# Optimization experiments

Hardware: AMD Instinct MI355X
Metric: run time of the kernel (lower is better)

Reference implementation:

```python
import jax, jax.numpy as jnp
import numpy as np

N_NODES = 10000
N_EDGES = 320000
D_IN = 256
D_OUT = 256
MAX_NORM = 0.95

def setup_inputs() -> dict:
    key = jax.random.key(0)
    ks = jax.random.split(key, 7)
    x = jax.random.normal(ks[0], (N_NODES, D_IN), dtype=jnp.float32)
    edge_index = jax.random.randint(ks[1], (2, N_EDGES), 0, N_NODES, dtype=jnp.int64)
    # xavier-ish scales
    W = jax.random.normal(ks[2], (D_OUT, D_IN), dtype=jnp.float32) * (1.0 / np.sqrt(D_IN))
    b = jax.random.normal(ks[3], (D_OUT,), dtype=jnp.float32) * 0.02
    mag_w = jax.random.normal(ks[4], (1, D_IN), dtype=jnp.float32) * 0.02
    mag_b = jax.random.normal(ks[5], (1,), dtype=jnp.float32) * 0.02
    attn_w = jax.random.normal(ks[6], (1, 2 * D_OUT), dtype=jnp.float32) * (1.0 / np.sqrt(2 * D_OUT))
    return {"x": x, "edge_index": edge_index, "W": W, "b": b,
            "mag_w": mag_w, "mag_b": mag_b, "attn_w": attn_w}

def _expmap0(u):
    # Poincare ball exp map at origin, curvature c = 1.0
    un = jnp.linalg.norm(u, axis=-1, keepdims=True)
    un_c = jnp.maximum(un, 1e-15)
    return jnp.tanh(un_c) * u / un_c

def reference(x, edge_index, W, b, mag_w, mag_b, attn_w):
    N = x.shape[0]
    F_out = W.shape[0]
    # linear transform + directional/magnitude decomposition
    h_raw = x @ W.T + b                                              # (N, F)
    h_dir = h_raw / jnp.maximum(jnp.linalg.norm(h_raw, axis=-1, keepdims=True), 1e-12)
    h_mag = jax.nn.sigmoid(x @ mag_w.T + mag_b) * 1.5                # (N, 1)
    h = h_dir * h_mag                                                # (N, F)
    src, tgt = edge_index[0], edge_index[1]
    h_src = h[src]                                                   # (E, F)
    h_tgt = h[tgt]                                                   # (E, F)
    # attn(cat([h_src, h_tgt])) == h_src @ a_s + h_tgt @ a_t (avoids concat)
    a_s, a_t = attn_w[0, :F_out], attn_w[0, F_out:]
    scores = h_src @ a_s + h_tgt @ a_t                               # (E,)
    # scatter softmax over edges grouped by target node
    mx = jnp.maximum(jax.ops.segment_max(scores, tgt, num_segments=N), -1e9)
    ex = jnp.exp(scores - mx[tgt])
    se = jax.ops.segment_sum(ex, tgt, num_segments=N)
    attn_weights = ex / (se[tgt] + 1e-10)                            # (E,)
    # weighted message aggregation
    agg = jax.ops.segment_sum(h_src * attn_weights[:, None], tgt, num_segments=N)
    h_combined = h + agg
    h_poincare = _expmap0(h_combined)
    norms = jnp.linalg.norm(h_poincare, axis=1, keepdims=True)
    return jnp.where(norms > MAX_NORM, h_poincare * (MAX_NORM / (norms + 1e-8)), h_poincare)
```

## Files before the change

kernel.cpp:

```cpp
#include <hip/hip_runtime.h>
#include <math.h>

#define N_NODES 10000
#define N_EDGES 320000
#define D 256
#define CAP 128
#define BM 32
#define LDK 40
#define GB_GEMM ((N_NODES + BM - 1) / BM)
#define GB_BUILD ((N_EDGES + 255) / 256)

typedef __attribute__((ext_vector_type(8))) short short8;
typedef __attribute__((ext_vector_type(4))) float f32x4;

__device__ __forceinline__ ushort f2bf(float f) {
    union { float f; unsigned u; } v; v.f = f;
    unsigned r = v.u + 0x7FFFu + ((v.u >> 16) & 1u);
    return (ushort)(r >> 16);
}
__device__ __forceinline__ float bf2f(ushort u) {
    union { unsigned u; float f; } v; v.u = (unsigned)u << 16;
    return v.f;
}

__global__ __launch_bounds__(256) void k_prep(const float* __restrict__ W,
                                              ushort* __restrict__ Wb,
                                              unsigned* __restrict__ deg) {
    const int tid = blockIdx.x * 256 + threadIdx.x;
    const int i = tid * 4;
    const float4 v = *(const float4*)&W[i];
    ushort4 o;
    o.x = f2bf(v.x); o.y = f2bf(v.y); o.z = f2bf(v.z); o.w = f2bf(v.w);
    *(ushort4*)&Wb[i] = o;
    if (tid < N_NODES) deg[tid] = 0u;
}

__global__ __launch_bounds__(256) void k_main(const float* __restrict__ x,
                                              const ushort* __restrict__ Wb,
                                              const float* __restrict__ b,
                                              const float* __restrict__ mag_w,
                                              const float* __restrict__ mag_b,
                                              const float* __restrict__ attn_w,
                                              const int* __restrict__ ei,
                                              unsigned* __restrict__ deg,
                                              int* __restrict__ csr_src,
                                              ushort* __restrict__ hb,
                                              float* __restrict__ es) {
    if (blockIdx.x >= GB_GEMM) {
        const int e = (blockIdx.x - GB_GEMM) * 256 + threadIdx.x;
        if (e < N_EDGES) {
            int src = ei[e];
            int tgt = ei[N_EDGES + e];
            src = min(max(src, 0), N_NODES - 1);
            tgt = min(max(tgt, 0), N_NODES - 1);
            const unsigned slot = atomicAdd(&deg[tgt], 1u);
            if (slot < CAP) csr_src[(size_t)tgt * CAP + slot] = src;
        }
        return;
    }

    __shared__ ushort ldsA[2][BM * LDK];
    __shared__ ushort ldsB[2][256 * LDK];
    __shared__ float red_ssq[4][BM], red_ra[4][BM];
    __shared__ float smrow[BM], scl[BM];

    const int t = threadIdx.x;
    const int w = t >> 6, l = t & 63;
    const int bm = blockIdx.x * BM;
    const int sra = t >> 3, ka = (t & 7) * 4;
    const int am = bm + sra;
    const int srb = t >> 2, kb = (t & 3) * 8;
    const int fl = l & 15;
    const int fh = (l >> 4) * 8;
    const int rq = (l >> 4) * 4;

    f32x4 acc[2][4];
#pragma unroll
    for (int r = 0; r < 2; ++r)
#pragma unroll
        for (int c = 0; c < 4; ++c) acc[r][c] = (f32x4)(0.f);
    float sm_part = 0.f;

    float4 xa;
    short8 bv[4];

    {
        xa = make_float4(0.f, 0.f, 0.f, 0.f);
        if (am < N_NODES) xa = *(const float4*)&x[(size_t)am * D + ka];
        const float4 mwv = *(const float4*)&mag_w[ka];
        sm_part += xa.x * mwv.x + xa.y * mwv.y + xa.z * mwv.z + xa.w * mwv.w;
#pragma unroll
        for (int p = 0; p < 4; ++p)
            bv[p] = *(const short8*)&Wb[(size_t)(p * 64 + srb) * D + kb];
        ushort4 av;
        av.x = f2bf(xa.x); av.y = f2bf(xa.y); av.z = f2bf(xa.z); av.w = f2bf(xa.w);
        *(ushort4*)&ldsA[0][sra * LDK + ka] = av;
#pragma unroll
        for (int p = 0; p < 4; ++p)
            *(short8*)&ldsB[0][(p * 64 + srb) * LDK + kb] = bv[p];
    }
    __syncthreads();

    int cur = 0;
    for (int k0 = 32; k0 < D; k0 += 32) {
        xa = make_float4(0.f, 0.f, 0.f, 0.f);
        if (am < N_NODES) xa = *(const float4*)&x[(size_t)am * D + k0 + ka];
        const float4 mwv = *(const float4*)&mag_w[k0 + ka];
        sm_part += xa.x * mwv.x + xa.y * mwv.y + xa.z * mwv.z + xa.w * mwv.w;
#pragma unroll
        for (int p = 0; p < 4; ++p)
            bv[p] = *(const short8*)&Wb[(size_t)(p * 64 + srb) * D + k0 + kb];

        short8 af[2], bfr[4];
#pragma unroll
        for (int r = 0; r < 2; ++r)
            af[r] = *(short8*)&ldsA[cur][(r * 16 + fl) * LDK + fh];
#pragma unroll
        for (int c = 0; c < 4; ++c)
            bfr[c] = *(short8*)&ldsB[cur][(w * 64 + c * 16 + fl) * LDK + fh];
#pragma unroll
        for (int r = 0; r < 2; ++r)
#pragma unroll
            for (int c = 0; c < 4; ++c)
                acc[r][c] = __builtin_amdgcn_mfma_f32_16x16x32_bf16(af[r], bfr[c], acc[r][c], 0, 0, 0);

        ushort4 av;
        av.x = f2bf(xa.x); av.y = f2bf(xa.y); av.z = f2bf(xa.z); av.w = f2bf(xa.w);
        *(ushort4*)&ldsA[cur ^ 1][sra * LDK + ka] = av;
#pragma unroll
        for (int p = 0; p < 4; ++p)
            *(short8*)&ldsB[cur ^ 1][(p * 64 + srb) * LDK + kb] = bv[p];
        __syncthreads();
        cur ^= 1;
    }
    {
        short8 af[2], bfr[4];
#pragma unroll
        for (int r = 0; r < 2; ++r)
            af[r] = *(short8*)&ldsA[cur][(r * 16 + fl) * LDK + fh];
#pragma unroll
        for (int c = 0; c < 4; ++c)
            bfr[c] = *(short8*)&ldsB[cur][(w * 64 + c * 16 + fl) * LDK + fh];
#pragma unroll
        for (int r = 0; r < 2; ++r)
#pragma unroll
            for (int c = 0; c < 4; ++c)
                acc[r][c] = __builtin_amdgcn_mfma_f32_16x16x32_bf16(af[r], bfr[c], acc[r][c], 0, 0, 0);
    }

#pragma unroll
    for (int o = 1; o < 8; o <<= 1) sm_part += __shfl_xor(sm_part, o);
    if ((t & 7) == 0) smrow[sra] = sm_part;

    float bn[4], asn[4];
#pragma unroll
    for (int c = 0; c < 4; ++c) {
        const int n = w * 64 + c * 16 + fl;
        bn[c]  = b[n];
        asn[c] = attn_w[n];
    }

#pragma unroll
    for (int r = 0; r < 2; ++r) {
#pragma unroll
        for (int reg = 0; reg < 4; ++reg) {
            float vssq = 0.f, vra = 0.f;
#pragma unroll
            for (int c = 0; c < 4; ++c) {
                const float v = acc[r][c][reg] + bn[c];
                vssq += v * v;
                vra  += v * asn[c];
            }
#pragma unroll
            for (int o = 1; o < 16; o <<= 1) {
                vssq += __shfl_xor(vssq, o);
                vra  += __shfl_xor(vra, o);
            }
            if (fl == 0) {
                const int m = r * 16 + rq + reg;
                red_ssq[w][m] = vssq;
                red_ra[w][m]  = vra;
            }
        }
    }
    __syncthreads();

    if (t < BM) {
        const int gm = bm + t;
        const float ssq = red_ssq[0][t] + red_ssq[1][t] + red_ssq[2][t] + red_ssq[3][t];
        const float ra  = red_ra[0][t]  + red_ra[1][t]  + red_ra[2][t]  + red_ra[3][t];
        const float norm = sqrtf(ssq);
        const float mag  = 1.5f / (1.f + expf(-(smrow[t] + mag_b[0])));
        const float scale = mag / fmaxf(norm, 1e-12f);
        scl[t] = scale;
        if (gm < N_NODES) es[gm] = expf(ra * scale);
    }
    __syncthreads();

#pragma unroll
    for (int r = 0; r < 2; ++r) {
#pragma unroll
        for (int reg = 0; reg < 4; ++reg) {
            const int ml = r * 16 + rq + reg;
            const int m = bm + ml;
            if (m < N_NODES) {
                const float scale = scl[ml];
#pragma unroll
                for (int c = 0; c < 4; ++c) {
                    const int n = w * 64 + c * 16 + fl;
                    hb[(size_t)m * D + n] = f2bf((acc[r][c][reg] + bn[c]) * scale);
                }
            }
        }
    }
}

__global__ __launch_bounds__(256) void k_agg(const ushort* __restrict__ hb,
                                             const unsigned* __restrict__ deg,
                                             const int* __restrict__ csr_src,
                                             const float* __restrict__ es,
                                             float* __restrict__ out) {
    const int wv = threadIdx.x >> 6;
    const int n = blockIdx.x * 4 + wv;
    const int lane = threadIdx.x & 63;
    const int d = min((int)deg[n], CAP);
    const size_t cbase = (size_t)n * CAP;

    int src0 = 0, src1 = 0;
    float w0 = 0.f, w1 = 0.f;
    if (lane < d)      { src0 = csr_src[cbase + lane];      w0 = es[src0]; }
    if (lane + 64 < d) { src1 = csr_src[cbase + lane + 64]; w1 = es[src1]; }
    float sum = w0 + w1;
#pragma unroll
    for (int o = 32; o > 0; o >>= 1) sum += __shfl_xor(sum, o);
    const float inv = 1.f / (sum + 1e-10f);

    const int coff = lane * 4;
    float4 A0 = make_float4(0.f, 0.f, 0.f, 0.f), A1 = A0, A2 = A0, A3 = A0;

    {
        const int cnt = min(d, 64);
        int e = 0;
        for (; e + 8 <= cnt; e += 8) {
            int s[8]; float q[8]; ushort4 v[8];
#pragma unroll
            for (int j = 0; j < 8; ++j) { s[j] = __shfl(src0, e + j); q[j] = __shfl(w0, e + j); }
#pragma unroll
            for (int j = 0; j < 8; ++j) v[j] = *(const ushort4*)&hb[(size_t)s[j] * D + coff];
#pragma unroll
            for (int j = 0; j < 8; ++j) {
                float4* A = (j & 2) ? ((j & 1) ? &A3 : &A2) : ((j & 1) ? &A1 : &A0);
                A->x += q[j] * bf2f(v[j].x); A->y += q[j] * bf2f(v[j].y);
                A->z += q[j] * bf2f(v[j].z); A->w += q[j] * bf2f(v[j].w);
            }
        }
        for (; e < cnt; ++e) {
            const int s0 = __shfl(src0, e);
            const float q0 = __shfl(w0, e);
            const ushort4 v0 = *(const ushort4*)&hb[(size_t)s0 * D + coff];
            A0.x += q0 * bf2f(v0.x); A0.y += q0 * bf2f(v0.y); A0.z += q0 * bf2f(v0.z); A0.w += q0 * bf2f(v0.w);
        }
    }
    if (d > 64) {
        const int cnt = d - 64;
        int e = 0;
        for (; e + 8 <= cnt; e += 8) {
            int s[8]; float q[8]; ushort4 v[8];
#pragma unroll
            for (int j = 0; j < 8; ++j) { s[j] = __shfl(src1, e + j); q[j] = __shfl(w1, e + j); }
#pragma unroll
            for (int j = 0; j < 8; ++j) v[j] = *(const ushort4*)&hb[(size_t)s[j] * D + coff];
#pragma unroll
            for (int j = 0; j < 8; ++j) {
                float4* A = (j & 2) ? ((j & 1) ? &A3 : &A2) : ((j & 1) ? &A1 : &A0);
                A->x += q[j] * bf2f(v[j].x); A->y += q[j] * bf2f(v[j].y);
                A->z += q[j] * bf2f(v[j].z); A->w += q[j] * bf2f(v[j].w);
            }
        }
        for (; e < cnt; ++e) {
            const int s0 = __shfl(src1, e);
            const float q0 = __shfl(w1, e);
            const ushort4 v0 = *(const ushort4*)&hb[(size_t)s0 * D + coff];
            A0.x += q0 * bf2f(v0.x); A0.y += q0 * bf2f(v0.y); A0.z += q0 * bf2f(v0.z); A0.w += q0 * bf2f(v0.w);
        }
    }
    float4 acc = make_float4((A0.x + A1.x + A2.x + A3.x) * inv,
                             (A0.y + A1.y + A2.y + A3.y) * inv,
                             (A0.z + A1.z + A2.z + A3.z) * inv,
                             (A0.w + A1.w + A2.w + A3.w) * inv);

    const ushort4 hnv = *(const ushort4*)&hb[(size_t)n * D + coff];
    float4 u = make_float4(bf2f(hnv.x) + acc.x, bf2f(hnv.y) + acc.y,
                           bf2f(hnv.z) + acc.z, bf2f(hnv.w) + acc.w);
    float ssq = u.x * u.x + u.y * u.y + u.z * u.z + u.w * u.w;
#pragma unroll
    for (int o = 32; o > 0; o >>= 1) ssq += __shfl_xor(ssq, o);
    const float un = sqrtf(ssq);
    const float un_c = fmaxf(un, 1e-15f);
    const float th = tanhf(un_c);
    float s = th / un_c;
    const float pn = th * (un / un_c);
    if (pn > 0.95f) s *= 0.95f / (pn + 1e-8f);
    float4 p = make_float4(u.x * s, u.y * s, u.z * s, u.w * s);
    *(float4*)&out[(size_t)n * D + coff] = p;
}

extern "C" void kernel_launch(void* const* d_in, const int* in_sizes, int n_in,
                              void* d_out, int out_size, void* d_ws, size_t ws_size,
                              hipStream_t stream) {
    const float* x      = (const float*)d_in[0];
    const int*   ei     = (const int*)d_in[1];
    const float* W      = (const float*)d_in[2];
    const float* b      = (const float*)d_in[3];
    const float* mag_w  = (const float*)d_in[4];
    const float* mag_b  = (const float*)d_in[5];
    const float* attn_w = (const float*)d_in[6];
    float* out = (float*)d_out;

    char* ws = (char*)d_ws;
    ushort* hb = (ushort*)ws;         ws += (size_t)N_NODES * D * sizeof(ushort);
    float* es = (float*)ws;           ws += (size_t)N_NODES * sizeof(float);
    unsigned* deg = (unsigned*)ws;    ws += (size_t)N_NODES * sizeof(unsigned);
    int* csr_src = (int*)ws;          ws += (size_t)N_NODES * CAP * sizeof(int);
    ushort* Wb = (ushort*)ws;         ws += (size_t)D * D * sizeof(ushort);

    k_prep<<<(D * D) / (256 * 4), 256, 0, stream>>>(W, Wb, deg);
    k_main<<<GB_GEMM + GB_BUILD, 256, 0, stream>>>(
        x, Wb, b, mag_w, mag_b, attn_w, ei, deg, csr_src, hb, es);
    k_agg<<<N_NODES / 4, 256, 0, stream>>>(hb, deg, csr_src, es, out);
}
```

Measured before the change: 57.63 us.

## Merge three kernels into two with in-kernel CSR build barrier

Drops the separate weight-conversion prep kernel: the GEMM now reads fp32 W directly and converts it to bf16 on the fly, while a few extra blocks zero the degree array. The CSR bucket build moves from the GEMM kernel into the aggregation kernel, where aggregation blocks spin on a global completion counter until all build blocks finish. This removes one launch and its dependency gap. In exchange, every GEMM block repeats the W conversion and reads twice the weight bytes. The spin-wait also depends on build blocks being scheduled before aggregation blocks, and it has a bounded guard to avoid deadlock.

```diff
diff --git a/kernel.cpp b/kernel.cpp
--- a/kernel.cpp
+++ b/kernel.cpp
@@ -7,8 +7,10 @@
 #define CAP 128
 #define BM 32
 #define LDK 40
+#define ZB 10
 #define GB_GEMM ((N_NODES + BM - 1) / BM)
 #define GB_BUILD ((N_EDGES + 255) / 256)
+#define N_AGG (N_NODES / 4)
 
 typedef __attribute__((ext_vector_type(8))) short short8;
 typedef __attribute__((ext_vector_type(4))) float f32x4;
@@ -22,40 +24,25 @@
     union { unsigned u; float f; } v; v.u = (unsigned)u << 16;
     return v.f;
 }
-
-__global__ __launch_bounds__(256) void k_prep(const float* __restrict__ W,
-                                              ushort* __restrict__ Wb,
-                                              unsigned* __restrict__ deg) {
-    const int tid = blockIdx.x * 256 + threadIdx.x;
-    const int i = tid * 4;
-    const float4 v = *(const float4*)&W[i];
-    ushort4 o;
-    o.x = f2bf(v.x); o.y = f2bf(v.y); o.z = f2bf(v.z); o.w = f2bf(v.w);
-    *(ushort4*)&Wb[i] = o;
-    if (tid < N_NODES) deg[tid] = 0u;
-}
-
-__global__ __launch_bounds__(256) void k_main(const float* __restrict__ x,
-                                              const ushort* __restrict__ Wb,
-                                              const float* __restrict__ b,
-                                              const float* __restrict__ mag_w,
-                                              const float* __restrict__ mag_b,
-                                              const float* __restrict__ attn_w,
-                                              const int* __restrict__ ei,
-                                              unsigned* __restrict__ deg,
-                                              int* __restrict__ csr_src,
-                                              ushort* __restrict__ hb,
-                                              float* __restrict__ es) {
-    if (blockIdx.x >= GB_GEMM) {
-        const int e = (blockIdx.x - GB_GEMM) * 256 + threadIdx.x;
-        if (e < N_EDGES) {
-            int src = ei[e];
-            int tgt = ei[N_EDGES + e];
-            src = min(max(src, 0), N_NODES - 1);
-            tgt = min(max(tgt, 0), N_NODES - 1);
-            const unsigned slot = atomicAdd(&deg[tgt], 1u);
-            if (slot < CAP) csr_src[(size_t)tgt * CAP + slot] = src;
-        }
+__device__ __forceinline__ short8 cvt8(const float4 a, const float4 b) {
+    short8 r;
+    r[0] = f2bf(a.x); r[1] = f2bf(a.y); r[2] = f2bf(a.z); r[3] = f2bf(a.w);
+    r[4] = f2bf(b.x); r[5] = f2bf(b.y); r[6] = f2bf(b.z); r[7] = f2bf(b.w);
+    return r;
+}
+
+__global__ __launch_bounds__(256) void k_front(const float* __restrict__ x,
+                                               const float* __restrict__ W,
+                                               const float* __restrict__ b,
+                                               const float* __restrict__ mag_w,
+                                               const float* __restrict__ mag_b,
+                                               const float* __restrict__ attn_w,
+                                               unsigned* __restrict__ deg,
+                                               ushort* __restrict__ hb,
+                                               float* __restrict__ es) {
+    if (blockIdx.x < ZB) {
+        for (int i = blockIdx.x * 256 + threadIdx.x; i <= N_NODES; i += ZB * 256)
+            deg[i] = 0u;
         return;
     }
 
@@ -66,7 +53,7 @@
 
     const int t = threadIdx.x;
     const int w = t >> 6, l = t & 63;
-    const int bm = blockIdx.x * BM;
+    const int bm = (blockIdx.x - ZB) * BM;
     const int sra = t >> 3, ka = (t & 7) * 4;
     const int am = bm + sra;
     const int srb = t >> 2, kb = (t & 3) * 8;
@@ -81,35 +68,37 @@
         for (int c = 0; c < 4; ++c) acc[r][c] = (f32x4)(0.f);
     float sm_part = 0.f;
 
-    float4 xa;
-    short8 bv[4];
-
     {
-        xa = make_float4(0.f, 0.f, 0.f, 0.f);
+        float4 xa = make_float4(0.f, 0.f, 0.f, 0.f);
         if (am < N_NODES) xa = *(const float4*)&x[(size_t)am * D + ka];
         const float4 mwv = *(const float4*)&mag_w[ka];
         sm_part += xa.x * mwv.x + xa.y * mwv.y + xa.z * mwv.z + xa.w * mwv.w;
-#pragma unroll
-        for (int p = 0; p < 4; ++p)
-            bv[p] = *(const short8*)&Wb[(size_t)(p * 64 + srb) * D + kb];
         ushort4 av;
         av.x = f2bf(xa.x); av.y = f2bf(xa.y); av.z = f2bf(xa.z); av.w = f2bf(xa.w);
         *(ushort4*)&ldsA[0][sra * LDK + ka] = av;
 #pragma unroll
-        for (int p = 0; p < 4; ++p)
-            *(short8*)&ldsB[0][(p * 64 + srb) * LDK + kb] = bv[p];
+        for (int p = 0; p < 4; ++p) {
+            const size_t row = (size_t)(p * 64 + srb) * D + kb;
+            const float4 w0 = *(const float4*)&W[row];
+            const float4 w1 = *(const float4*)&W[row + 4];
+            *(short8*)&ldsB[0][(p * 64 + srb) * LDK + kb] = cvt8(w0, w1);
+        }
     }
     __syncthreads();
 
     int cur = 0;
     for (int k0 = 32; k0 < D; k0 += 32) {
-        xa = make_float4(0.f, 0.f, 0.f, 0.f);
+        float4 xa = make_float4(0.f, 0.f, 0.f, 0.f);
         if (am < N_NODES) xa = *(const float4*)&x[(size_t)am * D + k0 + ka];
         const float4 mwv = *(const float4*)&mag_w[k0 + ka];
         sm_part += xa.x * mwv.x + xa.y * mwv.y + xa.z * mwv.z + xa.w * mwv.w;
-#pragma unroll
-        for (int p = 0; p < 4; ++p)
-            bv[p] = *(const short8*)&Wb[(size_t)(p * 64 + srb) * D + k0 + kb];
+        float4 wv[4][2];
+#pragma unroll
+        for (int p = 0; p < 4; ++p) {
+            const size_t row = (size_t)(p * 64 + srb) * D + k0 + kb;
+            wv[p][0] = *(const float4*)&W[row];
+            wv[p][1] = *(const float4*)&W[row + 4];
+        }
 
         short8 af[2], bfr[4];
 #pragma unroll
@@ -129,7 +118,7 @@
         *(ushort4*)&ldsA[cur ^ 1][sra * LDK + ka] = av;
 #pragma unroll
         for (int p = 0; p < 4; ++p)
-            *(short8*)&ldsB[cur ^ 1][(p * 64 + srb) * LDK + kb] = bv[p];
+            *(short8*)&ldsB[cur ^ 1][(p * 64 + srb) * LDK + kb] = cvt8(wv[p][0], wv[p][1]);
         __syncthreads();
         cur ^= 1;
     }
@@ -215,21 +204,63 @@
     }
 }
 
-__global__ __launch_bounds__(256) void k_agg(const ushort* __restrict__ hb,
-                                             const unsigned* __restrict__ deg,
-                                             const int* __restrict__ csr_src,
-                                             const float* __restrict__ es,
-                                             float* __restrict__ out) {
+__global__ __launch_bounds__(256) void k_back(const int* __restrict__ ei,
+                                              unsigned* __restrict__ deg,
+                                              int* __restrict__ csr_src,
+                                              const ushort* __restrict__ hb,
+                                              const float* __restrict__ es,
+                                              float* __restrict__ out) {
+    const int bid = blockIdx.x;
+    if (bid < GB_BUILD) {
+        const int e = bid * 256 + threadIdx.x;
+        if (e < N_EDGES) {
+            int src = ei[e];
+            int tgt = ei[N_EDGES + e];
+            src = min(max(src, 0), N_NODES - 1);
+            tgt = min(max(tgt, 0), N_NODES - 1);
+            const unsigned slot = atomicAdd(&deg[tgt], 1u);
+            if (slot < CAP)
+                __hip_atomic_store(&csr_src[(size_t)tgt * CAP + slot], src,
+                                   __ATOMIC_RELAXED, __HIP_MEMORY_SCOPE_AGENT);
+        }
+        __syncthreads();
+        if (threadIdx.x == 0)
+            __hip_atomic_fetch_add(&deg[N_NODES], 1u,
+                                   __ATOMIC_RELEASE, __HIP_MEMORY_SCOPE_AGENT);
+        return;
+    }
+
+    if (threadIdx.x == 0) {
+        int guard = 0;
+        while (__hip_atomic_load(&deg[N_NODES], __ATOMIC_ACQUIRE,
+                                 __HIP_MEMORY_SCOPE_AGENT) < (unsigned)GB_BUILD) {
+            __builtin_amdgcn_s_sleep(8);
+            if (++guard > (1 << 22)) break;
+        }
+    }
+    __syncthreads();
+
     const int wv = threadIdx.x >> 6;
-    const int n = blockIdx.x * 4 + wv;
+    const int n = (bid - GB_BUILD) * 4 + wv;
     const int lane = threadIdx.x & 63;
-    const int d = min((int)deg[n], CAP);
+    const int d = min((int)__hip_atomic_load(&deg[n], __ATOMIC_RELAXED,
+                                             __HIP_MEMORY_SCOPE_AGENT), CAP);
     const size_t cbase = (size_t)n * CAP;
 
     int src0 = 0, src1 = 0;
     float w0 = 0.f, w1 = 0.f;
-    if (lane < d)      { src0 = csr_src[cbase + lane];      w0 = es[src0]; }
-    if (lane + 64 < d) { src1 = csr_src[cbase + lane + 64]; w1 = es[src1]; }
+    if (lane < d) {
+        src0 = __hip_atomic_load(&csr_src[cbase + lane], __ATOMIC_RELAXED,
+                                 __HIP_MEMORY_SCOPE_AGENT);
+        src0 = min(max(src0, 0), N_NODES - 1);
+        w0 = es[src0];
+    }
+    if (lane + 64 < d) {
+        src1 = __hip_atomic_load(&csr_src[cbase + lane + 64], __ATOMIC_RELAXED,
+                                 __HIP_MEMORY_SCOPE_AGENT);
+        src1 = min(max(src1, 0), N_NODES - 1);
+        w1 = es[src1];
+    }
     float sum = w0 + w1;
 #pragma unroll
     for (int o = 32; o > 0; o >>= 1) sum += __shfl_xor(sum, o);
@@ -320,12 +351,10 @@
     char* ws = (char*)d_ws;
     ushort* hb = (ushort*)ws;         ws += (size_t)N_NODES * D * sizeof(ushort);
     float* es = (float*)ws;           ws += (size_t)N_NODES * sizeof(float);
-    unsigned* deg = (unsigned*)ws;    ws += (size_t)N_NODES * sizeof(unsigned);
+    unsigned* deg = (unsigned*)ws;    ws += (size_t)(N_NODES + 8) * sizeof(unsigned);
     int* csr_src = (int*)ws;          ws += (size_t)N_NODES * CAP * sizeof(int);
-    ushort* Wb = (ushort*)ws;         ws += (size_t)D * D * sizeof(ushort);
-
-    k_prep<<<(D * D) / (256 * 4), 256, 0, stream>>>(W, Wb, deg);
-    k_main<<<GB_GEMM + GB_BUILD, 256, 0, stream>>>(
-        x, Wb, b, mag_w, mag_b, attn_w, ei, deg, csr_src, hb, es);
-    k_agg<<<N_NODES / 4, 256, 0, stream>>>(hb, deg, csr_src, es, out);
-}
+
+    k_front<<<ZB + GB_GEMM, 256, 0, stream>>>(x, W, b, mag_w, mag_b, attn_w,
+                                              deg, hb, es);
+    k_back<<<GB_BUILD + N_AGG, 256, 0, stream>>>(ei, deg, csr_src, hb, es, out);
+}
```

Result: slower. 181.3 us (+214.5%).
